# Performance work log

Measured on AMD Instinct MI355X. Metric: run time of the kernel, lower is better.

Reference implementation:

```python
import jax, jax.numpy as jnp
import numpy as np

B, S, D = 32, 2048, 1024
TEMP = 9.0  # RelaxedBernoulli temperature (torch.tensor([9]))


def setup_inputs() -> dict:
    key = jax.random.key(0)
    ks = jax.random.split(key, 12)
    sd = 1.0 / np.sqrt(D)
    sd2 = 1.0 / np.sqrt(2 * D)
    return {
        "h_t": jax.random.normal(ks[0], (B, D), jnp.float32),
        "h_s": jax.random.normal(ks[1], (B, S, D), jnp.float32),
        "auxi_hs": jax.random.normal(ks[2], (B, S, D), jnp.float32),
        "noise_u": jax.random.uniform(ks[3], (B, S, 1), jnp.float32),
        # linear_map: Linear(2*dim, 1) with bias
        "Wmap": jax.random.normal(ks[4], (2 * D,), jnp.float32) * sd2,
        "bmap": jax.random.normal(ks[5], (), jnp.float32) * sd2,
        # mlp_h: Linear(dim, dim) + Tanh + Linear(dim, 1)
        "W1": jax.random.normal(ks[6], (D, D), jnp.float32) * sd,
        "b1": jax.random.normal(ks[7], (D,), jnp.float32) * sd,
        "W2": jax.random.normal(ks[8], (D,), jnp.float32) * sd,
        "b2": jax.random.normal(ks[9], (), jnp.float32) * sd,
        # linear_out: Linear(2*dim, dim, bias=False) (attn_type='dot')
        "Wout": jax.random.normal(ks[10], (D, 2 * D), jnp.float32) * sd2,
    }


def reference(h_t, h_s, auxi_hs, noise_u, Wmap, bmap, W1, b1, W2, b2, Wout):
    # h_t: (B, D) one-step query; h_s, auxi_hs: (B, S, D)
    d = h_s.shape[-1]
    # linear_map(concat(auxi_hs, H_t)) without materializing the (B,S,2D) concat
    Wm_a, Wm_t = Wmap[:d], Wmap[d:]
    logits_p = jnp.einsum('bsd,d->bs', auxi_hs, Wm_a) + (h_t @ Wm_t)[:, None] + bmap  # (B,S)
    logits_p = logits_p[..., None]  # (B,S,1); note logit(sigmoid(x)) == x
    # RelaxedBernoulli(temp=9, probs=sigmoid(logits_p)).sample() with explicit uniform noise
    eps = 1e-7
    u = jnp.clip(noise_u, eps, 1.0 - eps)
    logistic = jnp.log(u) - jnp.log1p(-u)  # (B,S,1)
    G = jax.nn.sigmoid((logits_p + logistic) / TEMP)  # (B,S,1)
    # mlp_h(h_s): Linear -> tanh -> Linear
    e = jnp.einsum('bsd,d->bs', jnp.tanh(jnp.einsum('bsd,ed->bse', h_s, W1) + b1), W2) + b2
    e = e[..., None]  # (B,S,1)
    # custom softmax: max over dim 0 (batch!), exp, gate
    v = jnp.max(e, axis=0, keepdims=True)  # (1,S,1)
    scores = jnp.exp(e - v) * G  # (B,S,1)
    align = scores[..., 0] / jnp.sum(scores[..., 0], axis=1, keepdims=True)  # (B,S)
    c = jnp.einsum('bs,bsd->bd', align, h_s)  # (B,D)
    attn_h = jnp.tanh(jnp.concatenate([c, h_t], axis=-1) @ Wout.T)  # (B,D)
    return attn_h, align
```

## Files before the change

kernel.cpp:

```cpp
#include <hip/hip_runtime.h>
#include <hip/hip_bf16.h>
#include <math.h>

#define B_ 32
#define S_ 2048
#define D_ 1024
#define TEMP_ 9.0f

typedef __attribute__((ext_vector_type(8))) short short8;
typedef __attribute__((ext_vector_type(4))) float f32x4;
typedef __attribute__((ext_vector_type(4))) unsigned short ushort4v;

__device__ __forceinline__ unsigned short f2b(float f) {
  union { float f; unsigned int u; } v; v.f = f;
  unsigned int r = v.u;
  r += 0x7fffu + ((r >> 16) & 1u);
  return (unsigned short)(r >> 16);
}
__device__ __forceinline__ float b2f(unsigned short b) {
  union { float f; unsigned int u; } v; v.u = ((unsigned int)b) << 16;
  return v.f;
}
__device__ __forceinline__ float tanh_fast(float x) {
  float ez = __expf(2.f * x);
  return 1.f - __fdividef(2.f, ez + 1.f);
}

#define GLOAD_LDS16(g, l) \
  __builtin_amdgcn_global_load_lds((const __attribute__((address_space(1))) void*)(g), \
                                   (__attribute__((address_space(3))) void*)(l), 16, 0, 0)

__global__ void k_conv(const float* __restrict__ src, unsigned short* __restrict__ dst, int n8) {
  int i = blockIdx.x * 256 + threadIdx.x;
  if (i >= n8) return;
  const float4* g = reinterpret_cast<const float4*>(src) + (size_t)i * 2;
  float4 x0 = g[0], x1 = g[1];
  uint4 w;
  w.x = f2b(x0.x) | ((unsigned)f2b(x0.y) << 16);
  w.y = f2b(x0.z) | ((unsigned)f2b(x0.w) << 16);
  w.z = f2b(x1.x) | ((unsigned)f2b(x1.y) << 16);
  w.w = f2b(x1.z) | ((unsigned)f2b(x1.w) << 16);
  reinterpret_cast<uint4*>(dst)[i] = w;
}

__global__ void k_pack_w1(const float* __restrict__ W1, unsigned short* __restrict__ w1t) {
  int c = blockIdx.x * 256 + threadIdx.x;
  int l  = c & 63;
  int kt = (c >> 6) & 31;
  int cg = c >> 11;
  int col = cg * 16 + (l & 15);
  int k0  = kt * 32 + (l >> 4) * 8;
  const float* src = W1 + (size_t)col * D_ + k0;
  float4 x0 = *reinterpret_cast<const float4*>(src);
  float4 x1 = *reinterpret_cast<const float4*>(src + 4);
  uint4 w;
  w.x = f2b(x0.x) | ((unsigned)f2b(x0.y) << 16);
  w.y = f2b(x0.z) | ((unsigned)f2b(x0.w) << 16);
  w.z = f2b(x1.x) | ((unsigned)f2b(x1.y) << 16);
  w.w = f2b(x1.z) | ((unsigned)f2b(x1.w) << 16);
  reinterpret_cast<uint4*>(w1t)[c] = w;
}

__global__ void k0_tdot(const float* __restrict__ h_t, const float* __restrict__ Wmap,
                        const float* __restrict__ bmap, float* __restrict__ tdot) {
  int b = blockIdx.x;
  int t = threadIdx.x;
  float p = 0.f;
  for (int k = t; k < D_; k += 256) p += h_t[b*D_ + k] * Wmap[D_ + k];
  __shared__ float red[256];
  red[t] = p; __syncthreads();
  for (int off = 128; off > 0; off >>= 1) { if (t < off) red[t] += red[t+off]; __syncthreads(); }
  if (t == 0) tdot[b] = red[0] + bmap[0];
}

__global__ void k1_gate(const float* __restrict__ aux, const float* __restrict__ Wmap,
                        const float* __restrict__ noise, const float* __restrict__ tdot,
                        float* __restrict__ Gout) {
  int w = (blockIdx.x * 256 + threadIdx.x) >> 6;
  int lane = threadIdx.x & 63;
  const float4* arow = reinterpret_cast<const float4*>(aux + (size_t)w * D_);
  const float4* wrow = reinterpret_cast<const float4*>(Wmap);
  float p = 0.f;
  for (int it = 0; it < 4; ++it) {
    float4 a = arow[it*64 + lane];
    float4 m = wrow[it*64 + lane];
    p += a.x*m.x + a.y*m.y + a.z*m.z + a.w*m.w;
  }
  for (int msk = 32; msk > 0; msk >>= 1) p += __shfl_xor(p, msk);
  if (lane == 0) {
    int b = w >> 11;
    float logits = p + tdot[b];
    float u = noise[w];
    u = fminf(fmaxf(u, 1e-7f), 1.f - 1e-7f);
    float logistic = logf(u) - log1pf(-u);
    float x = (logits + logistic) / TEMP_;
    Gout[w] = 1.f / (1.f + expf(-x));
  }
}

__device__ __forceinline__ void gate_rows(
    int bid, int wv, int lane,
    const float* __restrict__ aux, const float* __restrict__ Wmap,
    const float* __restrict__ noise, const float* __restrict__ tdot,
    float* __restrict__ Gout) {
  const float4* wrow = reinterpret_cast<const float4*>(Wmap);
  float4 m0 = wrow[lane], m1 = wrow[64 + lane], m2 = wrow[128 + lane], m3 = wrow[192 + lane];
  int rowG = (bid << 5) | (wv << 3);
#pragma unroll 2
  for (int i = 0; i < 8; ++i) {
    int row = rowG + i;
    const float4* arow = reinterpret_cast<const float4*>(aux + (size_t)row * D_);
    float4 a0 = arow[lane], a1 = arow[64 + lane], a2 = arow[128 + lane], a3 = arow[192 + lane];
    float p = a0.x*m0.x + a0.y*m0.y + a0.z*m0.z + a0.w*m0.w
            + a1.x*m1.x + a1.y*m1.y + a1.z*m1.z + a1.w*m1.w
            + a2.x*m2.x + a2.y*m2.y + a2.z*m2.z + a2.w*m2.w
            + a3.x*m3.x + a3.y*m3.y + a3.z*m3.z + a3.w*m3.w;
    for (int msk = 32; msk > 0; msk >>= 1) p += __shfl_xor(p, msk);
    if (lane == 0) {
      float logits = p + tdot[row >> 11];
      float u = noise[row];
      u = fminf(fmaxf(u, 1e-7f), 1.f - 1e-7f);
      float logistic = logf(u) - log1pf(-u);
      float x = (logits + logistic) / TEMP_;
      Gout[row] = 1.f / (1.f + expf(-x));
    }
  }
}

extern __shared__ unsigned short lds2[];

__global__ __launch_bounds__(256, 2) void k2gt(
    const unsigned short* __restrict__ Ag, const unsigned short* __restrict__ w1t,
    const float* __restrict__ b1, const float* __restrict__ W2,
    float* __restrict__ e_buf,
    const float* __restrict__ aux, const float* __restrict__ Wmap,
    const float* __restrict__ noise, const float* __restrict__ tdot,
    float* __restrict__ Gout) {
  int bid = blockIdx.x;
  int xcd = bid & 7;
  int sub = bid >> 3;
  int cc  = sub & 3;
  int rc  = xcd + 8 * (sub >> 2);
  int rowBase = rc * 128;
  int colBase = cc * 256;

  int t = threadIdx.x;
  int lane = t & 63;
  int wv = t >> 6;
  int kslot = lane >> 4;

  if ((bid >> 8) & 1) gate_rows(bid, wv, lane, aux, Wmap, noise, tdot, Gout);

  int aOff[8];
#pragma unroll
  for (int m = 0; m < 8; ++m) {
    int r = m * 16 + (lane & 15);
    aOff[m] = r * 64 + ((kslot ^ ((r >> 1) & 3)) << 4);
  }

  const unsigned short* gA[2];
  int dstA[2];
#pragma unroll
  for (int i = 0; i < 2; ++i) {
    int c = i * 256 + t;
    int r = c >> 2;
    int clog = (c & 3) ^ ((r >> 1) & 3);
    gA[i] = Ag + (size_t)(rowBase + r) * D_ + clog * 8;
    dstA[i] = c * 16;
  }

  const unsigned short* pB[4];
#pragma unroll
  for (int n = 0; n < 4; ++n) {
    int cg = (colBase >> 4) + wv * 4 + n;
    pB[n] = w1t + (size_t)cg * 16384 + lane * 8;
  }

  f32x4 acc[8][4] = {};
  short8 bfA[4], bfB[4];

#define STAGE(TT) do {                                                         \
    char* _ba = (char*)lds2 + ((TT) & 3) * 8192;                               \
    GLOAD_LDS16(gA[0] + (TT) * 32, _ba + dstA[0]);                             \
    GLOAD_LDS16(gA[1] + (TT) * 32, _ba + dstA[1]);                             \
  } while (0)

#define K2_TILE(T, VM, DO_B, DO_S, BFC, BFN) do {                              \
    asm volatile("s_waitcnt lgkmcnt(0)\n\ts_waitcnt vmcnt(" #VM ")" ::: "memory"); \
    __builtin_amdgcn_s_barrier();                                              \
    const char* _ab = (const char*)lds2 + ((T) & 3) * 8192;                    \
    short8 af[8];                                                              \
    _Pragma("unroll")                                                          \
    for (int m = 0; m < 8; ++m)                                                \
      af[m] = *reinterpret_cast<const short8*>(_ab + aOff[m]);                 \
    if (DO_B) {                                                                \
      _Pragma("unroll")                                                        \
      for (int n = 0; n < 4; ++n)                                              \
        BFN[n] = *reinterpret_cast<const short8*>(pB[n] + ((T) + 1) * 512);    \
    }                                                                          \
    if (DO_S) STAGE((T) + 3);                                                  \
    __builtin_amdgcn_s_setprio(1);                                             \
    _Pragma("unroll")                                                          \
    for (int m = 0; m < 8; ++m)                                                \
      _Pragma("unroll")                                                        \
      for (int n = 0; n < 4; ++n)                                              \
        acc[m][n] = __builtin_amdgcn_mfma_f32_16x16x32_bf16(af[m], BFC[n], acc[m][n], 0, 0, 0); \
    __builtin_amdgcn_s_setprio(0);                                             \
  } while (0)

  STAGE(0); STAGE(1); STAGE(2);
#pragma unroll
  for (int n = 0; n < 4; ++n)
    bfA[n] = *reinterpret_cast<const short8*>(pB[n]);

  K2_TILE(0, 0, true, true, bfA, bfB);
  K2_TILE(1, 2, true, true, bfB, bfA);
#pragma unroll
  for (int tt = 2; tt < 28; tt += 2) {
    K2_TILE(tt,     2, true, true, bfA, bfB);
    K2_TILE(tt + 1, 2, true, true, bfB, bfA);
  }
  K2_TILE(28, 2, true,  true,  bfA, bfB);
  K2_TILE(29, 2, true,  false, bfB, bfA);
  K2_TILE(30, 0, true,  false, bfA, bfB);
  K2_TILE(31, 0, false, false, bfB, bfA);
#undef K2_TILE
#undef STAGE

  float b1v[4], w2v[4];
#pragma unroll
  for (int n = 0; n < 4; ++n) {
    int col = colBase + wv * 64 + n * 16 + (lane & 15);
    b1v[n] = b1[col];
    w2v[n] = W2[col];
  }
#pragma unroll
  for (int m = 0; m < 8; ++m) {
#pragma unroll
    for (int j = 0; j < 4; ++j) {
      float s = 0.f;
#pragma unroll
      for (int n = 0; n < 4; ++n)
        s += tanh_fast(acc[m][n][j] + b1v[n]) * w2v[n];
      s += __shfl_xor(s, 1);
      s += __shfl_xor(s, 2);
      s += __shfl_xor(s, 4);
      s += __shfl_xor(s, 8);
      if ((lane & 15) == 0) {
        int row = rowBase + m * 16 + ((lane >> 4) << 2) + j;
        atomicAdd(&e_buf[row], s);
      }
    }
  }

  if (!((bid >> 8) & 1)) gate_rows(bid, wv, lane, aux, Wmap, noise, tdot, Gout);
}

#define BM 128
#define BN 128
#define BK 64
__global__ __launch_bounds__(256) void k2_egemm_f32(
    const float* __restrict__ h_s, const float* __restrict__ W1,
    const float* __restrict__ b1, const float* __restrict__ W2,
    float* __restrict__ e_buf) {
  __shared__ unsigned short As[BM * BK];
  __shared__ unsigned short Bs[BN * BK];
  int bid = blockIdx.x;
  int colBase = (bid & 7) * BN;
  int rowBase = (bid >> 3) * BM;
  int t = threadIdx.x;
  int lane = t & 63;
  int wave = t >> 6;
  int wr = wave >> 1, wc = wave & 1;
  f32x4 acc[4][4] = {};
  for (int k0 = 0; k0 < D_; k0 += BK) {
    __syncthreads();
    for (int i = 0; i < 4; ++i) {
      int flat = i*256 + t;
      int r = flat >> 3;
      int c8 = flat & 7;
      int byte = (r*128 + c8*16) ^ ((r & 7) << 4);
      {
        const float4* g = reinterpret_cast<const float4*>(h_s + (size_t)(rowBase + r)*D_ + k0 + c8*8);
        float4 x0 = g[0], x1 = g[1];
        uint4 w;
        w.x = f2b(x0.x) | ((unsigned)f2b(x0.y) << 16);
        w.y = f2b(x0.z) | ((unsigned)f2b(x0.w) << 16);
        w.z = f2b(x1.x) | ((unsigned)f2b(x1.y) << 16);
        w.w = f2b(x1.z) | ((unsigned)f2b(x1.w) << 16);
        *reinterpret_cast<uint4*>(reinterpret_cast<char*>(As) + byte) = w;
      }
      {
        const float4* g = reinterpret_cast<const float4*>(W1 + (size_t)(colBase + r)*D_ + k0 + c8*8);
        float4 x0 = g[0], x1 = g[1];
        uint4 w;
        w.x = f2b(x0.x) | ((unsigned)f2b(x0.y) << 16);
        w.y = f2b(x0.z) | ((unsigned)f2b(x0.w) << 16);
        w.z = f2b(x1.x) | ((unsigned)f2b(x1.y) << 16);
        w.w = f2b(x1.z) | ((unsigned)f2b(x1.w) << 16);
        *reinterpret_cast<uint4*>(reinterpret_cast<char*>(Bs) + byte) = w;
      }
    }
    __syncthreads();
    for (int kk = 0; kk < BK; kk += 32) {
      short8 af[4], bf[4];
      int kByte = kk*2 + ((lane >> 4) << 4);
      for (int m = 0; m < 4; ++m) {
        int r = wr*64 + m*16 + (lane & 15);
        int byte = (r*128 + kByte) ^ ((r & 7) << 4);
        af[m] = *reinterpret_cast<const short8*>(reinterpret_cast<const char*>(As) + byte);
      }
      for (int n = 0; n < 4; ++n) {
        int r = wc*64 + n*16 + (lane & 15);
        int byte = (r*128 + kByte) ^ ((r & 7) << 4);
        bf[n] = *reinterpret_cast<const short8*>(reinterpret_cast<const char*>(Bs) + byte);
      }
      for (int m = 0; m < 4; ++m)
        for (int n = 0; n < 4; ++n)
          acc[m][n] = __builtin_amdgcn_mfma_f32_16x16x32_bf16(af[m], bf[n], acc[m][n], 0, 0, 0);
    }
  }
  float b1v[4], w2v[4];
  for (int n = 0; n < 4; ++n) {
    int col = colBase + wc*64 + n*16 + (lane & 15);
    b1v[n] = b1[col];
    w2v[n] = W2[col];
  }
  for (int m = 0; m < 4; ++m) {
    for (int j = 0; j < 4; ++j) {
      float s = 0.f;
      for (int n = 0; n < 4; ++n)
        s += tanhf(acc[m][n][j] + b1v[n]) * w2v[n];
      s += __shfl_xor(s, 1);
      s += __shfl_xor(s, 2);
      s += __shfl_xor(s, 4);
      s += __shfl_xor(s, 8);
      if ((lane & 15) == 0) {
        int row = rowBase + wr*64 + m*16 + ((lane >> 4) << 2) + j;
        atomicAdd(&e_buf[row], s);
      }
    }
  }
}

__global__ void k3a_vmax(const float* __restrict__ e_buf, float* __restrict__ v) {
  int s = blockIdx.x * 256 + threadIdx.x;
  if (s >= S_) return;
  float m = -1e30f;
  for (int b = 0; b < B_; ++b) m = fmaxf(m, e_buf[b*S_ + s]);
  v[s] = m;
}

__global__ void k3b_align(const float* __restrict__ e_buf, const float* __restrict__ v,
                          float* __restrict__ galign) {
  int b = blockIdx.x;
  int t = threadIdx.x;
  __shared__ float sc[S_];
  __shared__ float red[256];
  float p = 0.f;
  for (int s = t; s < S_; s += 256) {
    float x = expf(e_buf[b*S_ + s] - v[s]) * galign[b*S_ + s];
    sc[s] = x;
    p += x;
  }
  red[t] = p; __syncthreads();
  for (int off = 128; off > 0; off >>= 1) { if (t < off) red[t] += red[t+off]; __syncthreads(); }
  float inv = 1.f / red[0];
  for (int s = t; s < S_; s += 256) galign[b*S_ + s] = sc[s] * inv;
}

__global__ void k4_ctx_bf16(const unsigned short* __restrict__ hsb, const float* __restrict__ align,
                            float* __restrict__ c) {
  int bid = blockIdx.x;
  int b = bid >> 6;
  int sBase = (bid & 63) * 32;
  int t = threadIdx.x;
  float4 accv = {0.f, 0.f, 0.f, 0.f};
  for (int si = 0; si < 32; ++si) {
    int s = sBase + si;
    float a = align[b*S_ + s];
    ushort4v hv = *reinterpret_cast<const ushort4v*>(hsb + (size_t)(b*S_ + s)*D_ + t*4);
    accv.x += a*b2f(hv.x); accv.y += a*b2f(hv.y); accv.z += a*b2f(hv.z); accv.w += a*b2f(hv.w);
  }
  atomicAdd(&c[b*D_ + t*4 + 0], accv.x);
  atomicAdd(&c[b*D_ + t*4 + 1], accv.y);
  atomicAdd(&c[b*D_ + t*4 + 2], accv.z);
  atomicAdd(&c[b*D_ + t*4 + 3], accv.w);
}

__global__ void k4_ctx_f32(const float* __restrict__ h_s, const float* __restrict__ align,
                           float* __restrict__ c) {
  int bid = blockIdx.x;
  int b = bid >> 6;
  int sBase = (bid & 63) * 32;
  int t = threadIdx.x;
  float4 accv = {0.f, 0.f, 0.f, 0.f};
  for (int si = 0; si < 32; ++si) {
    int s = sBase + si;
    float a = align[b*S_ + s];
    float4 hv = *reinterpret_cast<const float4*>(h_s + (size_t)(b*S_ + s)*D_ + t*4);
    accv.x += a*hv.x; accv.y += a*hv.y; accv.z += a*hv.z; accv.w += a*hv.w;
  }
  atomicAdd(&c[b*D_ + t*4 + 0], accv.x);
  atomicAdd(&c[b*D_ + t*4 + 1], accv.y);
  atomicAdd(&c[b*D_ + t*4 + 2], accv.z);
  atomicAdd(&c[b*D_ + t*4 + 3], accv.w);
}

__global__ void k5_out(const float* __restrict__ c, const float* __restrict__ h_t,
                       const float* __restrict__ Wout, float* __restrict__ out) {
  int W = (blockIdx.x * 256 + threadIdx.x) >> 6;
  int lane = threadIdx.x & 63;
  int b = W >> 10;
  int o = W & 1023;
  const float* wrow = Wout + (size_t)o * (2 * D_);
  float p = 0.f;
  for (int it = 0; it < 16; ++it) {
    int k = it*64 + lane;
    p += c[b*D_ + k] * wrow[k];
  }
  for (int it = 16; it < 32; ++it) {
    int k = it*64 + lane;
    p += h_t[b*D_ + (k - D_)] * wrow[k];
  }
  for (int m = 32; m > 0; m >>= 1) p += __shfl_xor(p, m);
  if (lane == 0) out[b*D_ + o] = tanhf(p);
}

extern "C" void kernel_launch(void* const* d_in, const int* in_sizes, int n_in,
                              void* d_out, int out_size, void* d_ws, size_t ws_size,
                              hipStream_t stream) {
  const float* h_t   = (const float*)d_in[0];
  const float* h_s   = (const float*)d_in[1];
  const float* aux   = (const float*)d_in[2];
  const float* noise = (const float*)d_in[3];
  const float* Wmap  = (const float*)d_in[4];
  const float* bmap  = (const float*)d_in[5];
  const float* W1    = (const float*)d_in[6];
  const float* b1    = (const float*)d_in[7];
  const float* W2    = (const float*)d_in[8];
  const float* Wout  = (const float*)d_in[10];

  float* out    = (float*)d_out;
  float* galign = out + B_*D_;

  const size_t HS_N   = (size_t)B_*S_*D_;
  const size_t W1_N   = (size_t)D_*D_;
  const size_t needed = HS_N*2 + W1_N*2 + (65536 + 32 + 2048 + 32768) * sizeof(float);

  if (ws_size >= needed) {
    unsigned short* hs_bf = (unsigned short*)d_ws;
    unsigned short* w1t   = hs_bf + HS_N;
    float* fws   = (float*)(w1t + W1_N);
    float* e_buf = fws;
    float* tdot  = fws + 65536;
    float* v     = fws + 65568;
    float* c     = fws + 67616;

    hipMemsetAsync(e_buf, 0, 65536 * sizeof(float), stream);
    hipMemsetAsync(c, 0, 32768 * sizeof(float), stream);

    hipFuncSetAttribute(reinterpret_cast<const void*>(k2gt),
                        hipFuncAttributeMaxDynamicSharedMemorySize, 32768);

    k_conv<<<(int)(HS_N/8/256), 256, 0, stream>>>(h_s, hs_bf, (int)(HS_N/8));
    k_pack_w1<<<512, 256, 0, stream>>>(W1, w1t);
    k0_tdot<<<32, 256, 0, stream>>>(h_t, Wmap, bmap, tdot);
    k2gt<<<2048, 256, 32768, stream>>>(hs_bf, w1t, b1, W2, e_buf,
                                       aux, Wmap, noise, tdot, galign);
    k3a_vmax<<<8, 256, 0, stream>>>(e_buf, v);
    k3b_align<<<32, 256, 0, stream>>>(e_buf, v, galign);
    k4_ctx_bf16<<<2048, 256, 0, stream>>>(hs_bf, galign, c);
    k5_out<<<8192, 256, 0, stream>>>(c, h_t, Wout, out);
  } else {
    float* ws    = (float*)d_ws;
    float* e_buf = ws;
    float* tdot  = ws + 65536;
    float* v     = ws + 65568;
    float* c     = ws + 67616;

    hipMemsetAsync(e_buf, 0, 65536 * sizeof(float), stream);
    hipMemsetAsync(c, 0, 32768 * sizeof(float), stream);

    k0_tdot<<<32, 256, 0, stream>>>(h_t, Wmap, bmap, tdot);
    k1_gate<<<16384, 256, 0, stream>>>(aux, Wmap, noise, tdot, galign);
    k2_egemm_f32<<<4096, 256, 0, stream>>>(h_s, W1, b1, W2, e_buf);
    k3a_vmax<<<8, 256, 0, stream>>>(e_buf, v);
    k3b_align<<<32, 256, 0, stream>>>(e_buf, v, galign);
    k4_ctx_f32<<<2048, 256, 0, stream>>>(h_s, galign, c);
    k5_out<<<8192, 256, 0, stream>>>(c, h_t, Wout, out);
  }
}
```

Baseline: 338.5 us.

## Fuse fp32-to-bf16 conversion of h_s into GEMM A-tile staging

Removes the separate k_conv pass that wrote a bf16 copy of h_s. The GEMM kernel now loads fp32 h_s into registers, converts with v_cvt_pk_bf16_f32, and writes the swizzled tiles to LDS through a double buffer. The context kernel reads fp32 h_s directly instead of the bf16 copy. This saves one full read plus a half-size write of h_s, at the cost of doubled GEMM A-side global traffic, a shallower prefetch pipeline (2 stages instead of 4), and direct register loads of W1 per tile instead of double-buffered prefetch.

```diff
diff --git a/kernel.cpp b/kernel.cpp
--- a/kernel.cpp
+++ b/kernel.cpp
@@ -21,26 +21,14 @@
   union { float f; unsigned int u; } v; v.u = ((unsigned int)b) << 16;
   return v.f;
 }
+__device__ __forceinline__ unsigned cvtpk(float a, float b) {
+  unsigned r;
+  asm("v_cvt_pk_bf16_f32 %0, %1, %2" : "=v"(r) : "v"(a), "v"(b));
+  return r;
+}
 __device__ __forceinline__ float tanh_fast(float x) {
   float ez = __expf(2.f * x);
   return 1.f - __fdividef(2.f, ez + 1.f);
-}
-
-#define GLOAD_LDS16(g, l) \
-  __builtin_amdgcn_global_load_lds((const __attribute__((address_space(1))) void*)(g), \
-                                   (__attribute__((address_space(3))) void*)(l), 16, 0, 0)
-
-__global__ void k_conv(const float* __restrict__ src, unsigned short* __restrict__ dst, int n8) {
-  int i = blockIdx.x * 256 + threadIdx.x;
-  if (i >= n8) return;
-  const float4* g = reinterpret_cast<const float4*>(src) + (size_t)i * 2;
-  float4 x0 = g[0], x1 = g[1];
-  uint4 w;
-  w.x = f2b(x0.x) | ((unsigned)f2b(x0.y) << 16);
-  w.y = f2b(x0.z) | ((unsigned)f2b(x0.w) << 16);
-  w.z = f2b(x1.x) | ((unsigned)f2b(x1.y) << 16);
-  w.w = f2b(x1.z) | ((unsigned)f2b(x1.w) << 16);
-  reinterpret_cast<uint4*>(dst)[i] = w;
 }
 
 __global__ void k_pack_w1(const float* __restrict__ W1, unsigned short* __restrict__ w1t) {
@@ -130,7 +118,7 @@
 extern __shared__ unsigned short lds2[];
 
 __global__ __launch_bounds__(256, 2) void k2gt(
-    const unsigned short* __restrict__ Ag, const unsigned short* __restrict__ w1t,
+    const float* __restrict__ h_s, const unsigned short* __restrict__ w1t,
     const float* __restrict__ b1, const float* __restrict__ W2,
     float* __restrict__ e_buf,
     const float* __restrict__ aux, const float* __restrict__ Wmap,
@@ -158,16 +146,12 @@
     aOff[m] = r * 64 + ((kslot ^ ((r >> 1) & 3)) << 4);
   }
 
-  const unsigned short* gA[2];
-  int dstA[2];
-#pragma unroll
-  for (int i = 0; i < 2; ++i) {
-    int c = i * 256 + t;
-    int r = c >> 2;
-    int clog = (c & 3) ^ ((r >> 1) & 3);
-    gA[i] = Ag + (size_t)(rowBase + r) * D_ + clog * 8;
-    dstA[i] = c * 16;
-  }
+  int r0 = t >> 2, r1 = 64 + (t >> 2);
+  int sl = t & 3;
+  const float* gS0 = h_s + (size_t)(rowBase + r0) * D_ + sl * 8;
+  const float* gS1 = h_s + (size_t)(rowBase + r1) * D_ + sl * 8;
+  int dstW0 = r0 * 64 + ((sl ^ ((r0 >> 1) & 3)) << 4);
+  int dstW1 = r1 * 64 + ((sl ^ ((r1 >> 1) & 3)) << 4);
 
   const unsigned short* pB[4];
 #pragma unroll
@@ -177,55 +161,61 @@
   }
 
   f32x4 acc[8][4] = {};
-  short8 bfA[4], bfB[4];
-
-#define STAGE(TT) do {                                                         \
-    char* _ba = (char*)lds2 + ((TT) & 3) * 8192;                               \
-    GLOAD_LDS16(gA[0] + (TT) * 32, _ba + dstA[0]);                             \
-    GLOAD_LDS16(gA[1] + (TT) * 32, _ba + dstA[1]);                             \
+  float4 sA0, sA1, sA2, sA3;
+
+#define LOADF(TT) do {                                                         \
+    sA0 = *reinterpret_cast<const float4*>(gS0 + (TT) * 32);                   \
+    sA1 = *reinterpret_cast<const float4*>(gS0 + (TT) * 32 + 4);               \
+    sA2 = *reinterpret_cast<const float4*>(gS1 + (TT) * 32);                   \
+    sA3 = *reinterpret_cast<const float4*>(gS1 + (TT) * 32 + 4);               \
   } while (0)
 
-#define K2_TILE(T, VM, DO_B, DO_S, BFC, BFN) do {                              \
-    asm volatile("s_waitcnt lgkmcnt(0)\n\ts_waitcnt vmcnt(" #VM ")" ::: "memory"); \
-    __builtin_amdgcn_s_barrier();                                              \
-    const char* _ab = (const char*)lds2 + ((T) & 3) * 8192;                    \
-    short8 af[8];                                                              \
+#define CVT_WRITE(TT) do {                                                     \
+    char* _bw = (char*)lds2 + ((TT) & 1) * 8192;                               \
+    uint4 w0, w1;                                                              \
+    w0.x = cvtpk(sA0.x, sA0.y); w0.y = cvtpk(sA0.z, sA0.w);                    \
+    w0.z = cvtpk(sA1.x, sA1.y); w0.w = cvtpk(sA1.z, sA1.w);                    \
+    w1.x = cvtpk(sA2.x, sA2.y); w1.y = cvtpk(sA2.z, sA2.w);                    \
+    w1.z = cvtpk(sA3.x, sA3.y); w1.w = cvtpk(sA3.z, sA3.w);                    \
+    *reinterpret_cast<uint4*>(_bw + dstW0) = w0;                               \
+    *reinterpret_cast<uint4*>(_bw + dstW1) = w1;                               \
+  } while (0)
+
+#define K2_TILE(T, DO_W, DO_L) do {                                            \
+    const char* _ab = (const char*)lds2 + ((T) & 1) * 8192;                    \
+    short8 af[8], bf[4];                                                       \
     _Pragma("unroll")                                                          \
     for (int m = 0; m < 8; ++m)                                                \
       af[m] = *reinterpret_cast<const short8*>(_ab + aOff[m]);                 \
-    if (DO_B) {                                                                \
-      _Pragma("unroll")                                                        \
-      for (int n = 0; n < 4; ++n)                                              \
-        BFN[n] = *reinterpret_cast<const short8*>(pB[n] + ((T) + 1) * 512);    \
-    }                                                                          \
-    if (DO_S) STAGE((T) + 3);                                                  \
+    _Pragma("unroll")                                                          \
+    for (int n = 0; n < 4; ++n)                                                \
+      bf[n] = *reinterpret_cast<const short8*>(pB[n] + (T) * 512);             \
+    if (DO_W) CVT_WRITE((T) + 1);                                              \
+    if (DO_L) LOADF((T) + 2);                                                  \
     __builtin_amdgcn_s_setprio(1);                                             \
     _Pragma("unroll")                                                          \
     for (int m = 0; m < 8; ++m)                                                \
       _Pragma("unroll")                                                        \
       for (int n = 0; n < 4; ++n)                                              \
-        acc[m][n] = __builtin_amdgcn_mfma_f32_16x16x32_bf16(af[m], BFC[n], acc[m][n], 0, 0, 0); \
+        acc[m][n] = __builtin_amdgcn_mfma_f32_16x16x32_bf16(af[m], bf[n], acc[m][n], 0, 0, 0); \
     __builtin_amdgcn_s_setprio(0);                                             \
+    asm volatile("s_waitcnt lgkmcnt(0)" ::: "memory");                         \
+    __builtin_amdgcn_s_barrier();                                              \
   } while (0)
 
-  STAGE(0); STAGE(1); STAGE(2);
-#pragma unroll
-  for (int n = 0; n < 4; ++n)
-    bfA[n] = *reinterpret_cast<const short8*>(pB[n]);
-
-  K2_TILE(0, 0, true, true, bfA, bfB);
-  K2_TILE(1, 2, true, true, bfB, bfA);
-#pragma unroll
-  for (int tt = 2; tt < 28; tt += 2) {
-    K2_TILE(tt,     2, true, true, bfA, bfB);
-    K2_TILE(tt + 1, 2, true, true, bfB, bfA);
-  }
-  K2_TILE(28, 2, true,  true,  bfA, bfB);
-  K2_TILE(29, 2, true,  false, bfB, bfA);
-  K2_TILE(30, 0, true,  false, bfA, bfB);
-  K2_TILE(31, 0, false, false, bfB, bfA);
+  LOADF(0);
+  CVT_WRITE(0);
+  LOADF(1);
+  asm volatile("s_waitcnt lgkmcnt(0)" ::: "memory");
+  __builtin_amdgcn_s_barrier();
+
+#pragma unroll
+  for (int tt = 0; tt < 30; ++tt) K2_TILE(tt, true, tt < 29);
+  K2_TILE(30, true, false);
+  K2_TILE(31, false, false);
 #undef K2_TILE
-#undef STAGE
+#undef CVT_WRITE
+#undef LOADF
 
   float b1v[4], w2v[4];
 #pragma unroll
@@ -369,25 +359,6 @@
   for (int s = t; s < S_; s += 256) galign[b*S_ + s] = sc[s] * inv;
 }
 
-__global__ void k4_ctx_bf16(const unsigned short* __restrict__ hsb, const float* __restrict__ align,
-                            float* __restrict__ c) {
-  int bid = blockIdx.x;
-  int b = bid >> 6;
-  int sBase = (bid & 63) * 32;
-  int t = threadIdx.x;
-  float4 accv = {0.f, 0.f, 0.f, 0.f};
-  for (int si = 0; si < 32; ++si) {
-    int s = sBase + si;
-    float a = align[b*S_ + s];
-    ushort4v hv = *reinterpret_cast<const ushort4v*>(hsb + (size_t)(b*S_ + s)*D_ + t*4);
-    accv.x += a*b2f(hv.x); accv.y += a*b2f(hv.y); accv.z += a*b2f(hv.z); accv.w += a*b2f(hv.w);
-  }
-  atomicAdd(&c[b*D_ + t*4 + 0], accv.x);
-  atomicAdd(&c[b*D_ + t*4 + 1], accv.y);
-  atomicAdd(&c[b*D_ + t*4 + 2], accv.z);
-  atomicAdd(&c[b*D_ + t*4 + 3], accv.w);
-}
-
 __global__ void k4_ctx_f32(const float* __restrict__ h_s, const float* __restrict__ align,
                            float* __restrict__ c) {
   int bid = blockIdx.x;
@@ -444,13 +415,11 @@
   float* out    = (float*)d_out;
   float* galign = out + B_*D_;
 
-  const size_t HS_N   = (size_t)B_*S_*D_;
   const size_t W1_N   = (size_t)D_*D_;
-  const size_t needed = HS_N*2 + W1_N*2 + (65536 + 32 + 2048 + 32768) * sizeof(float);
+  const size_t needed = W1_N*2 + (65536 + 32 + 2048 + 32768) * sizeof(float);
 
   if (ws_size >= needed) {
-    unsigned short* hs_bf = (unsigned short*)d_ws;
-    unsigned short* w1t   = hs_bf + HS_N;
+    unsigned short* w1t = (unsigned short*)d_ws;
     float* fws   = (float*)(w1t + W1_N);
     float* e_buf = fws;
     float* tdot  = fws + 65536;
@@ -461,16 +430,15 @@
     hipMemsetAsync(c, 0, 32768 * sizeof(float), stream);
 
     hipFuncSetAttribute(reinterpret_cast<const void*>(k2gt),
-                        hipFuncAttributeMaxDynamicSharedMemorySize, 32768);
-
-    k_conv<<<(int)(HS_N/8/256), 256, 0, stream>>>(h_s, hs_bf, (int)(HS_N/8));
+                        hipFuncAttributeMaxDynamicSharedMemorySize, 16384);
+
     k_pack_w1<<<512, 256, 0, stream>>>(W1, w1t);
     k0_tdot<<<32, 256, 0, stream>>>(h_t, Wmap, bmap, tdot);
-    k2gt<<<2048, 256, 32768, stream>>>(hs_bf, w1t, b1, W2, e_buf,
+    k2gt<<<2048, 256, 16384, stream>>>(h_s, w1t, b1, W2, e_buf,
                                        aux, Wmap, noise, tdot, galign);
     k3a_vmax<<<8, 256, 0, stream>>>(e_buf, v);
     k3b_align<<<32, 256, 0, stream>>>(e_buf, v, galign);
-    k4_ctx_bf16<<<2048, 256, 0, stream>>>(hs_bf, galign, c);
+    k4_ctx_f32<<<2048, 256, 0, stream>>>(h_s, galign, c);
     k5_out<<<8192, 256, 0, stream>>>(c, h_t, Wout, out);
   } else {
     float* ws    = (float*)d_ws;
```

Result: faster. 322.3 us (-4.8%).
